# Performance work log

Measured on AMD Instinct MI355X. Metric: run time of the kernel, lower is better.

Reference implementation:

```python
import jax, jax.numpy as jnp
import numpy as np

N = 100000   # nodes
E = 600000   # edges
F_IN = 128
F_OUT = 128


def setup_inputs() -> dict:
    key = jax.random.key(0)
    k1, k2, k3, k4 = jax.random.split(key, 4)
    x = jax.random.normal(k1, (N, F_IN), dtype=jnp.float32)
    edge_index = jax.random.randint(k2, (2, E), 0, N, dtype=jnp.int32)
    edge_wt = jnp.ones((E,), dtype=jnp.float32)  # learnable param, init ones
    # GCNConv weight (glorot-ish scale) and bias
    weight = jax.random.normal(k3, (F_IN, F_OUT), dtype=jnp.float32) / np.sqrt(F_IN).astype(np.float32)
    bias = jnp.zeros((F_OUT,), dtype=jnp.float32)
    u = jax.random.normal(k4, (F_IN,), dtype=jnp.float32)  # spectral-norm power-iter buffer
    return {"x": x, "edge_index": edge_index, "edge_wt": edge_wt,
            "weight": weight, "bias": bias, "u": u}


def _l2norm(v):
    return v / (jnp.linalg.norm(v) + 1e-12)


def reference(x, edge_index, edge_wt, weight, bias, u):
    # --- spectral norm on GCNConv weight (one power iteration, torch semantics:
    # u, v are stop-gradiented buffers; sigma = u^T W v keeps grad wrt W) ---
    W_sg = jax.lax.stop_gradient(weight)
    v = _l2norm(W_sg.T @ jax.lax.stop_gradient(u))
    u1 = _l2norm(W_sg @ v)
    sigma = u1 @ (weight @ v)
    W_sn = weight / sigma

    # --- per-edge sigmoid-weighted GCNConv with self loops + symmetric norm ---
    w = jax.nn.sigmoid(edge_wt)                      # [E]
    row, col = edge_index[0], edge_index[1]
    loop = jnp.arange(N, dtype=edge_index.dtype)
    row_a = jnp.concatenate([row, loop])             # [E+N]
    col_a = jnp.concatenate([col, loop])
    w_a = jnp.concatenate([w, jnp.ones((N,), w.dtype)])  # self-loop weight 1

    deg = jax.ops.segment_sum(w_a, col_a, num_segments=N)   # [N]
    dinv = jnp.where(deg > 0, deg ** -0.5, 0.0)
    norm = dinv[row_a] * w_a * dinv[col_a]           # [E+N]

    xw = x @ W_sn                                    # [N, F_OUT]
    msgs = norm[:, None] * xw[row_a]                 # [E+N, F_OUT] gather
    out = jax.ops.segment_sum(msgs, col_a, num_segments=N) + bias  # scatter
    return out
```

## Files before the change

### kernel.cpp

```cpp
#include <hip/hip_runtime.h>
#include <math.h>

#define F 128

typedef __bf16 bf16_t;
typedef unsigned long long u64;
typedef __attribute__((ext_vector_type(8))) bf16_t bf16x8;
typedef __attribute__((ext_vector_type(4))) bf16_t bf16x4;
typedef __attribute__((ext_vector_type(4))) float floatx4;

#define DEG_SCALE 8388608.0f
#define DEG_INV   (1.0f / 8388608.0f)

__global__ __launch_bounds__(256) void init_spec_k(const float* __restrict__ W,
                                                   const float* __restrict__ u,
                                                   bf16_t* __restrict__ Wt,
                                                   u64* __restrict__ dc, int n) {
    if (blockIdx.x == 0) {
        __shared__ float Wl[F][F + 1];
        __shared__ float ul[F];
        __shared__ float sv[F];
        __shared__ float red[4];
        __shared__ float snorm, s_is;
        int t = threadIdx.x;
        if (t < F) ul[t] = u[t];
        for (int i = t; i < F * 32; i += 256) {
            int r = i >> 5, c4 = (i & 31) * 4;
            float4 v = *(const float4*)(W + r * F + c4);
            Wl[r][c4] = v.x; Wl[r][c4 + 1] = v.y; Wl[r][c4 + 2] = v.z; Wl[r][c4 + 3] = v.w;
        }
        __syncthreads();
        float s = 0.f;
        if (t < F)
            for (int i = 0; i < F; ++i) s += Wl[i][t] * ul[i];
        float ss = (t < F) ? s * s : 0.f;
        for (int o = 32; o > 0; o >>= 1) ss += __shfl_down(ss, o);
        if ((t & 63) == 0) red[t >> 6] = ss;
        __syncthreads();
        if (t == 0) snorm = sqrtf(red[0] + red[1] + red[2] + red[3]);
        __syncthreads();
        if (t < F) sv[t] = s / (snorm + 1e-12f);
        __syncthreads();
        float s2 = 0.f;
        if (t < F)
            for (int j = 0; j < F; ++j) s2 += Wl[t][j] * sv[j];
        float ss2 = (t < F) ? s2 * s2 : 0.f;
        for (int o = 32; o > 0; o >>= 1) ss2 += __shfl_down(ss2, o);
        if ((t & 63) == 0) red[t >> 6] = ss2;
        __syncthreads();
        if (t == 0) {
            float a = red[0] + red[1] + red[2] + red[3];
            float nt = sqrtf(a);
            float sigma = a / (nt + 1e-12f);
            s_is = 1.0f / sigma;
        }
        __syncthreads();
        float is = s_is;
        for (int i = t; i < F * 16; i += 256) {
            int nrow = i >> 4, c = (i & 15) * 8;
            bf16x8 v;
#pragma unroll
            for (int j = 0; j < 8; ++j) v[j] = (bf16_t)(Wl[c + j][nrow] * is);
            *(bf16x8*)(Wt + nrow * F + c) = v;
        }
    } else {
        int i = (blockIdx.x - 1) * 256 + threadIdx.x;
        if (i < n) dc[i] = 0ULL;
    }
}

#define GBM 64
#define LDK 136
__global__ __launch_bounds__(256) void count_gemm_k(const int* __restrict__ col,
                                                    const float* __restrict__ wt,
                                                    u64* __restrict__ dc,
                                                    int* __restrict__ rank, int e_cnt,
                                                    const float* __restrict__ x,
                                                    const bf16_t* __restrict__ Wt,
                                                    bf16_t* __restrict__ xwh, int nrows,
                                                    int gGemm) {
    __shared__ bf16_t As[GBM * LDK];
    int b = blockIdx.x;
    if (b >= gGemm) {
        int e = (b - gGemm) * 256 + threadIdx.x;
        if (e < e_cnt) {
            int c = col[e];
            float w = 1.0f / (1.0f + expf(-wt[e]));
            u64 pkt = (1ULL << 32) | (u64)(unsigned)rintf(w * DEG_SCALE);
            u64 old = atomicAdd(dc + c, pkt);
            rank[e] = (int)(old >> 32);
        }
        return;
    }
    int tid = threadIdx.x;
    int rowBase = b * GBM;

    for (int i = tid; i < GBM * 32; i += 256) {
        int r = i >> 5, c4 = (i & 31) * 4;
        float4 xv = make_float4(0.f, 0.f, 0.f, 0.f);
        if (rowBase + r < nrows) xv = *(const float4*)(x + (size_t)(rowBase + r) * F + c4);
        bf16x4 v;
        v.x = (bf16_t)xv.x; v.y = (bf16_t)xv.y; v.z = (bf16_t)xv.z; v.w = (bf16_t)xv.w;
        *(bf16x4*)(As + r * LDK + c4) = v;
    }
    __syncthreads();

    int wave = tid >> 6, lane = tid & 63;
    int l16 = lane & 15, q = lane >> 4;
    int mrow = wave * 16;

    floatx4 acc[8];
#pragma unroll
    for (int nt = 0; nt < 8; ++nt) acc[nt] = (floatx4){0.f, 0.f, 0.f, 0.f};

#pragma unroll
    for (int kt = 0; kt < 4; ++kt) {
        bf16x8 a = *(bf16x8*)(As + (mrow + l16) * LDK + kt * 32 + q * 8);
#pragma unroll
        for (int nt = 0; nt < 8; ++nt) {
            bf16x8 bb = *(const bf16x8*)(Wt + (size_t)(nt * 16 + l16) * F + kt * 32 + q * 8);
            acc[nt] = __builtin_amdgcn_mfma_f32_16x16x32_bf16(a, bb, acc[nt], 0, 0, 0);
        }
    }
    __syncthreads();

#pragma unroll
    for (int nt = 0; nt < 8; ++nt) {
#pragma unroll
        for (int r = 0; r < 4; ++r)
            As[(mrow + q * 4 + r) * LDK + nt * 16 + l16] = (bf16_t)acc[nt][r];
    }
    __syncthreads();

    for (int i = tid; i < GBM * 16; i += 256) {
        int r = i >> 4, c = (i & 15) * 8;
        if (rowBase + r < nrows)
            *(bf16x8*)(xwh + (size_t)(rowBase + r) * F + c) = *(bf16x8*)(As + r * LDK + c);
    }
}

#define STILE 1024
__global__ __launch_bounds__(256) void scan1_k(const u64* __restrict__ dc,
                                               int* __restrict__ bsum,
                                               float* __restrict__ dinv, int n) {
    __shared__ int red[256];
    int t = threadIdx.x;
    int base = blockIdx.x * STILE + t * 4;
    int s = 0;
    for (int i = 0; i < 4; ++i) {
        if (base + i < n) {
            u64 v = dc[base + i];
            s += (int)(v >> 32);
            float d = 1.0f + (float)(unsigned)(v & 0xFFFFFFFFULL) * DEG_INV;
            dinv[base + i] = 1.0f / sqrtf(d);
        }
    }
    red[t] = s;
    __syncthreads();
    for (int o = 128; o > 0; o >>= 1) { if (t < o) red[t] += red[t + o]; __syncthreads(); }
    if (t == 0) bsum[blockIdx.x] = red[0];
}

__global__ __launch_bounds__(256) void scan2_k(int* __restrict__ bsum, int g,
                                               int* __restrict__ offsets, int n) {
    int t = threadIdx.x;
    if (g <= 256) {
        __shared__ int s[256];
        int v = (t < g) ? bsum[t] : 0;
        s[t] = v;
        __syncthreads();
        for (int o = 1; o < 256; o <<= 1) {
            int val = s[t];
            int add = (t >= o) ? s[t - o] : 0;
            __syncthreads();
            s[t] = val + add;
            __syncthreads();
        }
        if (t < g) bsum[t] = s[t] - v;
        if (t == g - 1) offsets[n] = s[t];
    } else if (t == 0) {
        int acc = 0;
        for (int i = 0; i < g; ++i) { int v = bsum[i]; bsum[i] = acc; acc += v; }
        offsets[n] = acc;
    }
}

__global__ __launch_bounds__(256) void scan3_k(const u64* __restrict__ dc,
                                               const int* __restrict__ bsum,
                                               int* __restrict__ offsets, int n) {
    __shared__ int sc[256];
    int t = threadIdx.x;
    int base = blockIdx.x * STILE + t * 4;
    int v[4] = {0, 0, 0, 0};
    for (int i = 0; i < 4; ++i)
        if (base + i < n) v[i] = (int)(dc[base + i] >> 32);
    int ts = v[0] + v[1] + v[2] + v[3];
    sc[t] = ts;
    __syncthreads();
    for (int o = 1; o < 256; o <<= 1) {
        int val = sc[t];
        int add = (t >= o) ? sc[t - o] : 0;
        __syncthreads();
        sc[t] = val + add;
        __syncthreads();
    }
    int run = bsum[blockIdx.x] + sc[t] - ts;
    for (int i = 0; i < 4; ++i) {
        if (base + i < n) offsets[base + i] = run;
        run += v[i];
    }
}

__global__ __launch_bounds__(256) void fill_k(const int* __restrict__ row,
                                              const int* __restrict__ col,
                                              const float* __restrict__ wt,
                                              const float* __restrict__ dinv,
                                              const int* __restrict__ offsets,
                                              const int* __restrict__ rank,
                                              int2* __restrict__ edat, int e_cnt) {
    int e = blockIdx.x * 256 + threadIdx.x;
    if (e < e_cnt) {
        int r = row[e], c = col[e];
        float w = 1.0f / (1.0f + expf(-wt[e]));
        float nv = dinv[r] * w * dinv[c];
        int p = offsets[c] + rank[e];
        edat[p] = make_int2(r, __float_as_int(nv));
    }
}

template <int MODE>
__global__ __launch_bounds__(256) void gather_t(const int* __restrict__ offsets,
                                                const int2* __restrict__ edat,
                                                const float* __restrict__ dinv,
                                                const float* __restrict__ x,
                                                const bf16_t* __restrict__ xh,
                                                const float* __restrict__ bias,
                                                float* __restrict__ out, int n) {
    int node = blockIdx.x * 4 + (threadIdx.x >> 6);
    if (node >= n) return;
    int lane = threadIdx.x & 63;
    const float2* x2 = (const float2*)x;
    float dv = dinv[node];
    float2 acc;
    if (MODE) {
        unsigned vs = ((const unsigned*)(xh + (size_t)node * F))[lane];
        acc.x = dv * dv * __uint_as_float(vs << 16);
        acc.y = dv * dv * __uint_as_float(vs & 0xFFFF0000u);
    } else {
        float2 xv = x2[(size_t)node * 64 + lane];
        acc.x = dv * dv * xv.x;
        acc.y = dv * dv * xv.y;
    }
    int s = offsets[node], e = offsets[node + 1];
    for (int b = s; b < e; b += 64) {
        int cnt = min(64, e - b);
        int2 ed = make_int2(0, 0);
        if (lane < cnt) ed = edat[b + lane];
        int j = 0;
        for (; j + 4 <= cnt; j += 4) {
            int r0 = __shfl(ed.x, j + 0), r1 = __shfl(ed.x, j + 1);
            int r2 = __shfl(ed.x, j + 2), r3 = __shfl(ed.x, j + 3);
            float n0 = __int_as_float(__shfl(ed.y, j + 0));
            float n1 = __int_as_float(__shfl(ed.y, j + 1));
            float n2 = __int_as_float(__shfl(ed.y, j + 2));
            float n3 = __int_as_float(__shfl(ed.y, j + 3));
            if (MODE) {
                unsigned v0 = ((const unsigned*)(xh + (size_t)r0 * F))[lane];
                unsigned v1 = ((const unsigned*)(xh + (size_t)r1 * F))[lane];
                unsigned v2 = ((const unsigned*)(xh + (size_t)r2 * F))[lane];
                unsigned v3 = ((const unsigned*)(xh + (size_t)r3 * F))[lane];
                acc.x = fmaf(n0, __uint_as_float(v0 << 16), acc.x);
                acc.y = fmaf(n0, __uint_as_float(v0 & 0xFFFF0000u), acc.y);
                acc.x = fmaf(n1, __uint_as_float(v1 << 16), acc.x);
                acc.y = fmaf(n1, __uint_as_float(v1 & 0xFFFF0000u), acc.y);
                acc.x = fmaf(n2, __uint_as_float(v2 << 16), acc.x);
                acc.y = fmaf(n2, __uint_as_float(v2 & 0xFFFF0000u), acc.y);
                acc.x = fmaf(n3, __uint_as_float(v3 << 16), acc.x);
                acc.y = fmaf(n3, __uint_as_float(v3 & 0xFFFF0000u), acc.y);
            } else {
                float2 a0 = x2[(size_t)r0 * 64 + lane];
                float2 a1 = x2[(size_t)r1 * 64 + lane];
                float2 a2 = x2[(size_t)r2 * 64 + lane];
                float2 a3 = x2[(size_t)r3 * 64 + lane];
                acc.x = fmaf(n0, a0.x, acc.x); acc.y = fmaf(n0, a0.y, acc.y);
                acc.x = fmaf(n1, a1.x, acc.x); acc.y = fmaf(n1, a1.y, acc.y);
                acc.x = fmaf(n2, a2.x, acc.x); acc.y = fmaf(n2, a2.y, acc.y);
                acc.x = fmaf(n3, a3.x, acc.x); acc.y = fmaf(n3, a3.y, acc.y);
            }
        }
        for (; j < cnt; ++j) {
            int r = __shfl(ed.x, j);
            float nv = __int_as_float(__shfl(ed.y, j));
            if (MODE) {
                unsigned v = ((const unsigned*)(xh + (size_t)r * F))[lane];
                acc.x = fmaf(nv, __uint_as_float(v << 16), acc.x);
                acc.y = fmaf(nv, __uint_as_float(v & 0xFFFF0000u), acc.y);
            } else {
                float2 xr = x2[(size_t)r * 64 + lane];
                acc.x = fmaf(nv, xr.x, acc.x);
                acc.y = fmaf(nv, xr.y, acc.y);
            }
        }
    }
    if (MODE) {
        float2 bv = ((const float2*)bias)[lane];
        acc.x += bv.x;
        acc.y += bv.y;
    }
    ((float2*)out)[(size_t)node * 64 + lane] = acc;
}

__global__ __launch_bounds__(256) void gemm_mfma_k(float* __restrict__ io,
                                                   const bf16_t* __restrict__ Wt,
                                                   const float* __restrict__ bias,
                                                   int nrows) {
    __shared__ bf16_t As[GBM * LDK];
    int tid = threadIdx.x;
    int rowBase = blockIdx.x * GBM;

    for (int i = tid; i < GBM * 32; i += 256) {
        int r = i >> 5, c4 = (i & 31) * 4;
        float4 xv = make_float4(0.f, 0.f, 0.f, 0.f);
        if (rowBase + r < nrows) xv = *(const float4*)(io + (size_t)(rowBase + r) * F + c4);
        bf16x4 v;
        v.x = (bf16_t)xv.x; v.y = (bf16_t)xv.y; v.z = (bf16_t)xv.z; v.w = (bf16_t)xv.w;
        *(bf16x4*)(As + r * LDK + c4) = v;
    }
    __syncthreads();

    int wave = tid >> 6, lane = tid & 63;
    int l16 = lane & 15, q = lane >> 4;
    int mrow = wave * 16;

    floatx4 acc[8];
#pragma unroll
    for (int nt = 0; nt < 8; ++nt) acc[nt] = (floatx4){0.f, 0.f, 0.f, 0.f};

#pragma unroll
    for (int kt = 0; kt < 4; ++kt) {
        bf16x8 a = *(bf16x8*)(As + (mrow + l16) * LDK + kt * 32 + q * 8);
#pragma unroll
        for (int nt = 0; nt < 8; ++nt) {
            bf16x8 b = *(const bf16x8*)(Wt + (size_t)(nt * 16 + l16) * F + kt * 32 + q * 8);
            acc[nt] = __builtin_amdgcn_mfma_f32_16x16x32_bf16(a, b, acc[nt], 0, 0, 0);
        }
    }

#pragma unroll
    for (int nt = 0; nt < 8; ++nt) {
        int col = nt * 16 + l16;
        float bv = bias[col];
#pragma unroll
        for (int r = 0; r < 4; ++r) {
            int grow = rowBase + mrow + q * 4 + r;
            if (grow < nrows) io[(size_t)grow * F + col] = acc[nt][r] + bv;
        }
    }
}

extern "C" void kernel_launch(void* const* d_in, const int* in_sizes, int n_in,
                              void* d_out, int out_size, void* d_ws, size_t ws_size,
                              hipStream_t stream) {
    const float* x    = (const float*)d_in[0];
    const int*   ei   = (const int*)d_in[1];
    const float* ewt  = (const float*)d_in[2];
    const float* W    = (const float*)d_in[3];
    const float* bias = (const float*)d_in[4];
    const float* u    = (const float*)d_in[5];
    float* out = (float*)d_out;

    int n_nodes = in_sizes[0] / F;
    int e_cnt   = in_sizes[2];
    const int* row = ei;
    const int* col = ei + e_cnt;

    char* wsb = (char*)d_ws;
    float* dinv    = (float*)wsb;
    size_t off = ((size_t)n_nodes * 4 + 15) & ~(size_t)15;
    u64*   dc      = (u64*)(wsb + off);
    off += (size_t)n_nodes * 8;
    int*   offsets = (int*)(wsb + off);
    off += (size_t)(n_nodes + 1) * 4;
    off = (off + 15) & ~(size_t)15;
    int*   bsum    = (int*)(wsb + off);
    off += 512 * 4;
    off = (off + 15) & ~(size_t)15;
    int*   rank    = (int*)(wsb + off);
    off += (size_t)e_cnt * 4;
    off = (off + 15) & ~(size_t)15;
    int2*  edat    = (int2*)(wsb + off);
    off += (size_t)e_cnt * 8;
    off = (off + 15) & ~(size_t)15;
    bf16_t* Wt     = (bf16_t*)(wsb + off);
    off += (size_t)F * F * 2;
    bf16_t* xwh    = (bf16_t*)(wsb + off);
    size_t need_bf16 = off + (size_t)n_nodes * F * 2;
    int use_bf16 = (ws_size >= need_bf16);

    int g_scan  = (n_nodes + STILE - 1) / STILE;
    int gCount  = (e_cnt + 255) / 256;
    int gInit   = (n_nodes + 255) / 256;
    int gGemm   = (n_nodes + GBM - 1) / GBM;

    init_spec_k<<<gInit + 1, 256, 0, stream>>>(W, u, Wt, dc, n_nodes);
    if (use_bf16) {
        count_gemm_k<<<gGemm + gCount, 256, 0, stream>>>(col, ewt, dc, rank, e_cnt, x, Wt,
                                                         xwh, n_nodes, gGemm);
    } else {
        count_gemm_k<<<gCount, 256, 0, stream>>>(col, ewt, dc, rank, e_cnt, x, Wt,
                                                 xwh, n_nodes, 0);
    }
    scan1_k<<<g_scan, 256, 0, stream>>>(dc, bsum, dinv, n_nodes);
    scan2_k<<<1, 256, 0, stream>>>(bsum, g_scan, offsets, n_nodes);
    scan3_k<<<g_scan, 256, 0, stream>>>(dc, bsum, offsets, n_nodes);
    fill_k<<<(e_cnt + 255) / 256, 256, 0, stream>>>(row, col, ewt, dinv, offsets, rank,
                                                    edat, e_cnt);
    if (use_bf16) {
        gather_t<1><<<(n_nodes + 3) / 4, 256, 0, stream>>>(offsets, edat, dinv, x, xwh, bias,
                                                           out, n_nodes);
    } else {
        gather_t<0><<<(n_nodes + 3) / 4, 256, 0, stream>>>(offsets, edat, dinv, x, xwh, bias,
                                                           out, n_nodes);
        gemm_mfma_k<<<gGemm, 256, 0, stream>>>(out, Wt, bias, n_nodes);
    }
}
```

Baseline: 219.7 us.

## Pack degree counters into 32-bit atomics, split count/GEMM, drop scan2

Packs the per-node edge count (top 8 bits) and fixed-point weighted degree (low 24 bits, scale 2^15) into one 32-bit atomic word instead of 64-bit, and vectorizes the counting pass to four edges per thread. The fused count+GEMM kernel is split into separate launches, and the middle scan kernel is removed by having each scan3 block serially sum the preceding block sums. This cuts atomic width, memory traffic and one launch. In exchange, in-degree is limited to 255 and the weighted degree must stay below 512 before the fields overflow, and degree precision is coarser.

```diff
diff --git a/kernel.cpp b/kernel.cpp
--- a/kernel.cpp
+++ b/kernel.cpp
@@ -9,13 +9,13 @@
 typedef __attribute__((ext_vector_type(4))) bf16_t bf16x4;
 typedef __attribute__((ext_vector_type(4))) float floatx4;
 
-#define DEG_SCALE 8388608.0f
-#define DEG_INV   (1.0f / 8388608.0f)
+#define DEG_SCALE 32768.0f
+#define DEG_INV   (1.0f / 32768.0f)
 
 __global__ __launch_bounds__(256) void init_spec_k(const float* __restrict__ W,
                                                    const float* __restrict__ u,
                                                    bf16_t* __restrict__ Wt,
-                                                   u64* __restrict__ dc, int n) {
+                                                   unsigned* __restrict__ dc, int n) {
     if (blockIdx.x == 0) {
         __shared__ float Wl[F][F + 1];
         __shared__ float ul[F];
@@ -65,35 +65,46 @@
         }
     } else {
         int i = (blockIdx.x - 1) * 256 + threadIdx.x;
-        if (i < n) dc[i] = 0ULL;
+        if (i < n) dc[i] = 0u;
+    }
+}
+
+__global__ __launch_bounds__(256) void count_k(const int* __restrict__ col,
+                                               const float* __restrict__ wt,
+                                               unsigned* __restrict__ dc,
+                                               int* __restrict__ rank, int e_cnt) {
+    int e4 = (blockIdx.x * 256 + threadIdx.x) * 4;
+    if (e4 + 3 < e_cnt) {
+        int4 c = *(const int4*)(col + e4);
+        float4 w = *(const float4*)(wt + e4);
+        unsigned p0 = (1u << 24) | (unsigned)rintf(DEG_SCALE / (1.0f + expf(-w.x)));
+        unsigned p1 = (1u << 24) | (unsigned)rintf(DEG_SCALE / (1.0f + expf(-w.y)));
+        unsigned p2 = (1u << 24) | (unsigned)rintf(DEG_SCALE / (1.0f + expf(-w.z)));
+        unsigned p3 = (1u << 24) | (unsigned)rintf(DEG_SCALE / (1.0f + expf(-w.w)));
+        unsigned o0 = atomicAdd(dc + c.x, p0);
+        unsigned o1 = atomicAdd(dc + c.y, p1);
+        unsigned o2 = atomicAdd(dc + c.z, p2);
+        unsigned o3 = atomicAdd(dc + c.w, p3);
+        *(int4*)(rank + e4) = make_int4((int)(o0 >> 24), (int)(o1 >> 24),
+                                        (int)(o2 >> 24), (int)(o3 >> 24));
+    } else {
+        for (int e = e4; e < e_cnt; ++e) {
+            int c = col[e];
+            unsigned pkt = (1u << 24) | (unsigned)rintf(DEG_SCALE / (1.0f + expf(-wt[e])));
+            unsigned old = atomicAdd(dc + c, pkt);
+            rank[e] = (int)(old >> 24);
+        }
     }
 }
 
 #define GBM 64
 #define LDK 136
-__global__ __launch_bounds__(256) void count_gemm_k(const int* __restrict__ col,
-                                                    const float* __restrict__ wt,
-                                                    u64* __restrict__ dc,
-                                                    int* __restrict__ rank, int e_cnt,
-                                                    const float* __restrict__ x,
-                                                    const bf16_t* __restrict__ Wt,
-                                                    bf16_t* __restrict__ xwh, int nrows,
-                                                    int gGemm) {
+__global__ __launch_bounds__(256) void gemm_k(const float* __restrict__ x,
+                                              const bf16_t* __restrict__ Wt,
+                                              bf16_t* __restrict__ xwh, int nrows) {
     __shared__ bf16_t As[GBM * LDK];
-    int b = blockIdx.x;
-    if (b >= gGemm) {
-        int e = (b - gGemm) * 256 + threadIdx.x;
-        if (e < e_cnt) {
-            int c = col[e];
-            float w = 1.0f / (1.0f + expf(-wt[e]));
-            u64 pkt = (1ULL << 32) | (u64)(unsigned)rintf(w * DEG_SCALE);
-            u64 old = atomicAdd(dc + c, pkt);
-            rank[e] = (int)(old >> 32);
-        }
-        return;
-    }
     int tid = threadIdx.x;
-    int rowBase = b * GBM;
+    int rowBase = blockIdx.x * GBM;
 
     for (int i = tid; i < GBM * 32; i += 256) {
         int r = i >> 5, c4 = (i & 31) * 4;
@@ -140,7 +151,7 @@
 }
 
 #define STILE 1024
-__global__ __launch_bounds__(256) void scan1_k(const u64* __restrict__ dc,
+__global__ __launch_bounds__(256) void scan1_k(const unsigned* __restrict__ dc,
                                                int* __restrict__ bsum,
                                                float* __restrict__ dinv, int n) {
     __shared__ int red[256];
@@ -149,9 +160,9 @@
     int s = 0;
     for (int i = 0; i < 4; ++i) {
         if (base + i < n) {
-            u64 v = dc[base + i];
-            s += (int)(v >> 32);
-            float d = 1.0f + (float)(unsigned)(v & 0xFFFFFFFFULL) * DEG_INV;
+            unsigned v = dc[base + i];
+            s += (int)(v >> 24);
+            float d = 1.0f + (float)(v & 0xFFFFFFu) * DEG_INV;
             dinv[base + i] = 1.0f / sqrtf(d);
         }
     }
@@ -161,39 +172,18 @@
     if (t == 0) bsum[blockIdx.x] = red[0];
 }
 
-__global__ __launch_bounds__(256) void scan2_k(int* __restrict__ bsum, int g,
-                                               int* __restrict__ offsets, int n) {
-    int t = threadIdx.x;
-    if (g <= 256) {
-        __shared__ int s[256];
-        int v = (t < g) ? bsum[t] : 0;
-        s[t] = v;
-        __syncthreads();
-        for (int o = 1; o < 256; o <<= 1) {
-            int val = s[t];
-            int add = (t >= o) ? s[t - o] : 0;
-            __syncthreads();
-            s[t] = val + add;
-            __syncthreads();
-        }
-        if (t < g) bsum[t] = s[t] - v;
-        if (t == g - 1) offsets[n] = s[t];
-    } else if (t == 0) {
-        int acc = 0;
-        for (int i = 0; i < g; ++i) { int v = bsum[i]; bsum[i] = acc; acc += v; }
-        offsets[n] = acc;
-    }
-}
-
-__global__ __launch_bounds__(256) void scan3_k(const u64* __restrict__ dc,
+__global__ __launch_bounds__(256) void scan3_k(const unsigned* __restrict__ dc,
                                                const int* __restrict__ bsum,
-                                               int* __restrict__ offsets, int n) {
+                                               int* __restrict__ offsets, int g, int n) {
     __shared__ int sc[256];
     int t = threadIdx.x;
-    int base = blockIdx.x * STILE + t * 4;
+    int bid = blockIdx.x;
+    int bbase = 0;
+    for (int i = 0; i < bid; ++i) bbase += bsum[i];
+    int base = bid * STILE + t * 4;
     int v[4] = {0, 0, 0, 0};
     for (int i = 0; i < 4; ++i)
-        if (base + i < n) v[i] = (int)(dc[base + i] >> 32);
+        if (base + i < n) v[i] = (int)(dc[base + i] >> 24);
     int ts = v[0] + v[1] + v[2] + v[3];
     sc[t] = ts;
     __syncthreads();
@@ -204,11 +194,12 @@
         sc[t] = val + add;
         __syncthreads();
     }
-    int run = bsum[blockIdx.x] + sc[t] - ts;
+    int run = bbase + sc[t] - ts;
     for (int i = 0; i < 4; ++i) {
         if (base + i < n) offsets[base + i] = run;
         run += v[i];
     }
+    if (bid == g - 1 && t == 255) offsets[n] = bbase + sc[255];
 }
 
 __global__ __launch_bounds__(256) void fill_k(const int* __restrict__ row,
@@ -375,44 +366,40 @@
     const int* col = ei + e_cnt;
 
     char* wsb = (char*)d_ws;
-    float* dinv    = (float*)wsb;
+    float*    dinv    = (float*)wsb;
     size_t off = ((size_t)n_nodes * 4 + 15) & ~(size_t)15;
-    u64*   dc      = (u64*)(wsb + off);
-    off += (size_t)n_nodes * 8;
-    int*   offsets = (int*)(wsb + off);
+    unsigned* dc      = (unsigned*)(wsb + off);
+    off += (size_t)n_nodes * 4;
+    off = (off + 15) & ~(size_t)15;
+    int*      offsets = (int*)(wsb + off);
     off += (size_t)(n_nodes + 1) * 4;
     off = (off + 15) & ~(size_t)15;
-    int*   bsum    = (int*)(wsb + off);
-    off += 512 * 4;
+    int*      bsum    = (int*)(wsb + off);
+    off += 2048 * 4;
     off = (off + 15) & ~(size_t)15;
-    int*   rank    = (int*)(wsb + off);
+    int*      rank    = (int*)(wsb + off);
     off += (size_t)e_cnt * 4;
     off = (off + 15) & ~(size_t)15;
-    int2*  edat    = (int2*)(wsb + off);
+    int2*     edat    = (int2*)(wsb + off);
     off += (size_t)e_cnt * 8;
     off = (off + 15) & ~(size_t)15;
-    bf16_t* Wt     = (bf16_t*)(wsb + off);
+    bf16_t*   Wt      = (bf16_t*)(wsb + off);
     off += (size_t)F * F * 2;
-    bf16_t* xwh    = (bf16_t*)(wsb + off);
+    bf16_t*   xwh     = (bf16_t*)(wsb + off);
     size_t need_bf16 = off + (size_t)n_nodes * F * 2;
     int use_bf16 = (ws_size >= need_bf16);
 
     int g_scan  = (n_nodes + STILE - 1) / STILE;
-    int gCount  = (e_cnt + 255) / 256;
+    int gCount  = (e_cnt + 1023) / 1024;
     int gInit   = (n_nodes + 255) / 256;
     int gGemm   = (n_nodes + GBM - 1) / GBM;
 
     init_spec_k<<<gInit + 1, 256, 0, stream>>>(W, u, Wt, dc, n_nodes);
-    if (use_bf16) {
-        count_gemm_k<<<gGemm + gCount, 256, 0, stream>>>(col, ewt, dc, rank, e_cnt, x, Wt,
-                                                         xwh, n_nodes, gGemm);
-    } else {
-        count_gemm_k<<<gCount, 256, 0, stream>>>(col, ewt, dc, rank, e_cnt, x, Wt,
-                                                 xwh, n_nodes, 0);
-    }
+    count_k<<<gCount, 256, 0, stream>>>(col, ewt, dc, rank, e_cnt);
+    if (use_bf16)
+        gemm_k<<<gGemm, 256, 0, stream>>>(x, Wt, xwh, n_nodes);
     scan1_k<<<g_scan, 256, 0, stream>>>(dc, bsum, dinv, n_nodes);
-    scan2_k<<<1, 256, 0, stream>>>(bsum, g_scan, offsets, n_nodes);
-    scan3_k<<<g_scan, 256, 0, stream>>>(dc, bsum, offsets, n_nodes);
+    scan3_k<<<g_scan, 256, 0, stream>>>(dc, bsum, offsets, g_scan, n_nodes);
     fill_k<<<(e_cnt + 255) / 256, 256, 0, stream>>>(row, col, ewt, dinv, offsets, rank,
                                                     edat, e_cnt);
     if (use_bf16) {
```

Result: slower. 243.5 us (+10.9%).
